# Kernel tuning notes

Measured on AMD Instinct MI355X. Metric: run time of the kernel, lower is better.

## Reference

```python
import jax, jax.numpy as jnp
import numpy as np

B, S_SPARSE, N_NUM, VOCAB = 512, 7, 6, 100
D, H, DFF, L = 1024, 16, 4096, 4
DH = D // 2  # 512, numeric encoding width
HD = D // H  # head dim 64
EPS = 1e-5


def setup_inputs() -> dict:
    key = jax.random.key(0)
    ks = jax.random.split(key, 16)
    inp = {
        'sparse': jax.random.randint(ks[0], (B, S_SPARSE), 0, VOCAB, dtype=jnp.int64),
        'numeric': jax.random.randint(ks[1], (B, N_NUM), 0, 100000, dtype=jnp.int32),
        'sparse_emb': jax.random.normal(ks[2], (VOCAB, D), jnp.float32),
        'numeric_emb': jax.random.normal(ks[3], (N_NUM, DH), jnp.float32),
        'Wqkv': jax.random.normal(ks[4], (L, 3 * D, D), jnp.float32) * 0.02,
        'bqkv': jnp.zeros((L, 3 * D), jnp.float32),
        'Wo': jax.random.normal(ks[5], (L, D, D), jnp.float32) * 0.02,
        'bo': jnp.zeros((L, D), jnp.float32),
        'W1': jax.random.normal(ks[6], (L, DFF, D), jnp.float32) * 0.02,
        'b1': jnp.zeros((L, DFF), jnp.float32),
        'W2': jax.random.normal(ks[7], (L, D, DFF), jnp.float32) * 0.02,
        'b2': jnp.zeros((L, D), jnp.float32),
        'ln1_g': jnp.ones((L, D), jnp.float32), 'ln1_b': jnp.zeros((L, D), jnp.float32),
        'ln2_g': jnp.ones((L, D), jnp.float32), 'ln2_b': jnp.zeros((L, D), jnp.float32),
    }
    return inp


def _ln(x, g, b):
    m = jnp.mean(x, -1, keepdims=True)
    v = jnp.mean((x - m) ** 2, -1, keepdims=True)
    return (x - m) * jax.lax.rsqrt(v + EPS) * g + b


def _encode_numeric(numeric):
    # piecewise-linear (thermometer) encoding, vectorized over batch & features
    mins = jnp.zeros((N_NUM,), jnp.float32)
    maxs = jnp.array([DH, DH, 100000.0, 100000.0, 100000.0, 100000.0], jnp.float32)
    scaled = (numeric.astype(jnp.float32) - mins) / (maxs - mins) * DH  # [B, 6]
    return jnp.clip(scaled[..., None] - jnp.arange(DH, dtype=jnp.float32), 0.0, 1.0)  # [B,6,DH]


def reference(sparse, numeric, sparse_emb, numeric_emb, Wqkv, bqkv, Wo, bo,
              W1, b1, W2, b2, ln1_g, ln1_b, ln2_g, ln2_b):
    enc = _encode_numeric(numeric)  # [B,6,DH]
    num_tok = jnp.concatenate(
        [enc, jnp.broadcast_to(numeric_emb[None], (sparse.shape[0], N_NUM, DH))], axis=2)  # [B,6,D]
    x = jnp.concatenate([sparse_emb[sparse], num_tok], axis=1)  # [B,13,D]

    scale = 1.0 / np.sqrt(HD)
    for l in range(L):
        qkv = jnp.einsum('bsd,ed->bse', x, Wqkv[l]) + bqkv[l]
        q, k, v = jnp.split(qkv, 3, axis=-1)
        bsz, s = x.shape[0], x.shape[1]
        q = q.reshape(bsz, s, H, HD)
        k = k.reshape(bsz, s, H, HD)
        v = v.reshape(bsz, s, H, HD)
        attn = jax.nn.softmax(jnp.einsum('bqhd,bkhd->bhqk', q, k) * scale, axis=-1)
        o = jnp.einsum('bhqk,bkhd->bqhd', attn, v).reshape(bsz, s, D)
        o = jnp.einsum('bsd,ed->bse', o, Wo[l]) + bo[l]
        x = _ln(x + o, ln1_g[l], ln1_b[l])  # post-norm
        h = jax.nn.gelu(jnp.einsum('bsd,fd->bsf', x, W1[l]) + b1[l], approximate=False)
        ff = jnp.einsum('bsf,df->bsd', h, W2[l]) + b2[l]
        x = _ln(x + ff, ln2_g[l], ln2_b[l])
    return x
```

## Files before the change

### kernel.cpp

```cpp
#include <hip/hip_runtime.h>
#include <hip/hip_bf16.h>
#include <cstdint>
#include <cmath>


typedef __bf16 bf16x8 __attribute__((ext_vector_type(8)));
typedef float  f32x4  __attribute__((ext_vector_type(4)));

__device__ __forceinline__ void async16(void* lds, const void* g) {
  __builtin_amdgcn_global_load_lds(
      (const __attribute__((address_space(1))) unsigned int*)g,
      (__attribute__((address_space(3))) unsigned int*)lds, 16, 0, 0);
}

__global__ __launch_bounds__(256) void f2b_kernel(const float* __restrict__ s,
                                                  __bf16* __restrict__ d, int n8) {
  int i = blockIdx.x * 256 + threadIdx.x;
  if (i >= n8) return;
  const float4* s4 = (const float4*)s;
  float4 a = s4[2 * i], b = s4[2 * i + 1];
  bf16x8 o;
  o[0] = (__bf16)a.x; o[1] = (__bf16)a.y; o[2] = (__bf16)a.z; o[3] = (__bf16)a.w;
  o[4] = (__bf16)b.x; o[5] = (__bf16)b.y; o[6] = (__bf16)b.z; o[7] = (__bf16)b.w;
  *(bf16x8*)(d + (size_t)i * 8) = o;
}

__global__ __launch_bounds__(256) void f2b2_kernel(
    const float* __restrict__ s0, __bf16* __restrict__ d0, int n0,
    const float* __restrict__ s1, __bf16* __restrict__ d1, int n8) {
  int i = blockIdx.x * 256 + threadIdx.x;
  if (i >= n8) return;
  const float* s; __bf16* d; int j;
  if (i < n0) { s = s0; d = d0; j = i; } else { s = s1; d = d1; j = i - n0; }
  const float4* s4 = (const float4*)s;
  float4 a = s4[2 * j], b = s4[2 * j + 1];
  bf16x8 o;
  o[0] = (__bf16)a.x; o[1] = (__bf16)a.y; o[2] = (__bf16)a.z; o[3] = (__bf16)a.w;
  o[4] = (__bf16)b.x; o[5] = (__bf16)b.y; o[6] = (__bf16)b.z; o[7] = (__bf16)b.w;
  *(bf16x8*)(d + (size_t)j * 8) = o;
}

__global__ __launch_bounds__(256) void build_x_kernel(
    const int* __restrict__ sparse, const int* __restrict__ numeric,
    const float* __restrict__ semb, const float* __restrict__ nemb,
    float* __restrict__ xf, __bf16* __restrict__ xb) {
  int r = blockIdx.x;
  int b = r / 13, s = r % 13;
  int t = threadIdx.x;
  size_t base = (size_t)r * 1024;
  if (s < 7) {
    int tok = sparse[b * 7 + s];
    const float* src = semb + (size_t)tok * 1024;
    for (int d = t; d < 1024; d += 256) {
      float v = src[d];
      xf[base + d] = v; xb[base + d] = (__bf16)v;
    }
  } else {
    int j = s - 7;
    float nv = (float)numeric[b * 6 + j];
    float scaled = nv * (j < 2 ? 1.0f : 512.0f / 100000.0f);
    for (int d = t; d < 1024; d += 256) {
      float v;
      if (d < 512) v = fminf(fmaxf(scaled - (float)d, 0.0f), 1.0f);
      else         v = nemb[j * 512 + (d - 512)];
      xf[base + d] = v; xb[base + d] = (__bf16)v;
    }
  }
}

template <int EPI>
__global__ __launch_bounds__(256) void gemm_bt(
    const __bf16* __restrict__ A, const __bf16* __restrict__ Bw,
    const float* __restrict__ bias, float* __restrict__ Cf,
    __bf16* __restrict__ Cb, int N, int K) {
  __shared__ __attribute__((aligned(16))) __bf16 As[128 * 64];
  __shared__ __attribute__((aligned(16))) __bf16 Bs[128 * 64];
  const int t = threadIdx.x;
  const int bm = blockIdx.x, bn = blockIdx.y;
  const int lane = t & 63, wid = t >> 6;
  const int wm = (wid >> 1) << 6, wn = (wid & 1) << 6;
  const int lm = lane & 15, lq = lane >> 4;
  const int srow = t >> 3, sp = t & 7;
  const int sc = sp ^ (srow & 7);
  const __bf16* Ag = A + (size_t)(bm * 128 + srow) * K + sc * 8;
  const __bf16* Bg = Bw + (size_t)(bn * 128 + srow) * K + sc * 8;
  const size_t rstep = (size_t)32 * K;
  f32x4 acc[4][4] = {};
  const int nIter = K >> 6;
  for (int k0 = 0; k0 < nIter; ++k0) {
    __syncthreads();
#pragma unroll
    for (int r = 0; r < 4; ++r) {
      async16(As + r * 2048 + t * 8, Ag + r * rstep);
      async16(Bs + r * 2048 + t * 8, Bg + r * rstep);
    }
    Ag += 64; Bg += 64;
    asm volatile("s_waitcnt vmcnt(0)" ::: "memory");
    __syncthreads();
#pragma unroll
    for (int kk = 0; kk < 2; ++kk) {
      bf16x8 af[4], bf[4];
#pragma unroll
      for (int i = 0; i < 4; i++) {
        int row = wm + i * 16 + lm;
        int pc = ((kk << 2) + lq) ^ (lm & 7);
        af[i] = *(const bf16x8*)(As + row * 64 + pc * 8);
      }
#pragma unroll
      for (int i = 0; i < 4; i++) {
        int row = wn + i * 16 + lm;
        int pc = ((kk << 2) + lq) ^ (lm & 7);
        bf[i] = *(const bf16x8*)(Bs + row * 64 + pc * 8);
      }
#pragma unroll
      for (int mi = 0; mi < 4; mi++)
#pragma unroll
        for (int ni = 0; ni < 4; ni++)
          acc[mi][ni] = __builtin_amdgcn_mfma_f32_16x16x32_bf16(af[mi], bf[ni], acc[mi][ni], 0, 0, 0);
    }
  }
  const int row0 = bm * 128 + wm + lq * 4;
  const int col0 = bn * 128 + wn + lm;
#pragma unroll
  for (int mi = 0; mi < 4; mi++) {
#pragma unroll
    for (int ni = 0; ni < 4; ni++) {
      int col = col0 + ni * 16;
      float bv = bias[col];
#pragma unroll
      for (int r = 0; r < 4; r++) {
        int row = row0 + mi * 16 + r;
        float v = acc[mi][ni][r] + bv;
        if (EPI == 2) {
          float u = fabsf(v);
          float y = 0.7978845608f * u * (1.0f + 0.044715f * u * u);
          float e = __expf(-2.0f * y);
          float th = (1.0f - e) * __builtin_amdgcn_rcpf(1.0f + e);
          v = 0.5f * v * (1.0f + (v < 0.0f ? -th : th));
        }
        if (EPI == 0) Cf[(size_t)row * N + col] = v;
        else          Cb[(size_t)row * N + col] = (__bf16)v;
      }
    }
  }
}

__global__ __launch_bounds__(64) void attn_kernel(const __bf16* __restrict__ qkv,
                                                  __bf16* __restrict__ o) {
  int bh = blockIdx.x;
  int b = bh >> 4, h = bh & 15;
  int lane = threadIdx.x;
  __shared__ float qs[13][68], ks[13][68], vs[13][68];
  __shared__ float S[13][16];
  const __bf16* base = qkv + (size_t)b * 13 * 3072 + h * 64 + lane;
#pragma unroll
  for (int i = 0; i < 13; i++) {
    qs[i][lane] = (float)base[(size_t)i * 3072];
    ks[i][lane] = (float)base[(size_t)i * 3072 + 1024];
    vs[i][lane] = (float)base[(size_t)i * 3072 + 2048];
  }
  __syncthreads();
  for (int rep = 0; rep < 3; rep++) {
    int idx = lane + rep * 64;
    if (idx < 169) {
      int i = idx / 13, j = idx % 13;
      float s = 0.f;
#pragma unroll
      for (int d = 0; d < 64; d++) s += qs[i][d] * ks[j][d];
      S[i][j] = s * 0.125f;
    }
  }
  __syncthreads();
  if (lane < 13) {
    float m = S[lane][0];
#pragma unroll
    for (int j = 1; j < 13; j++) m = fmaxf(m, S[lane][j]);
    float sum = 0.f;
#pragma unroll
    for (int j = 0; j < 13; j++) { float e = expf(S[lane][j] - m); S[lane][j] = e; sum += e; }
    float inv = 1.0f / sum;
#pragma unroll
    for (int j = 0; j < 13; j++) S[lane][j] *= inv;
  }
  __syncthreads();
  __bf16* ob = o + (size_t)b * 13 * 1024 + h * 64 + lane;
#pragma unroll
  for (int i = 0; i < 13; i++) {
    float s = 0.f;
#pragma unroll
    for (int j = 0; j < 13; j++) s += S[i][j] * vs[j][lane];
    ob[(size_t)i * 1024] = (__bf16)s;
  }
}

__global__ __launch_bounds__(256) void add_ln_kernel(
    const float* __restrict__ xin, const float* __restrict__ delta,
    const float* __restrict__ g, const float* __restrict__ bta,
    float* __restrict__ xf_out, __bf16* __restrict__ xb_out) {
  int r = blockIdx.x, t = threadIdx.x;
  size_t base = (size_t)r * 1024;
  float vals[4], s = 0.f, s2 = 0.f;
#pragma unroll
  for (int i = 0; i < 4; i++) {
    int d = t + i * 256;
    float v = xin[base + d] + delta[base + d];
    vals[i] = v; s += v; s2 += v * v;
  }
  __shared__ float red[8];
  for (int off = 32; off > 0; off >>= 1) { s += __shfl_down(s, off); s2 += __shfl_down(s2, off); }
  if ((t & 63) == 0) { red[t >> 6] = s; red[4 + (t >> 6)] = s2; }
  __syncthreads();
  float S1 = red[0] + red[1] + red[2] + red[3];
  float S2 = red[4] + red[5] + red[6] + red[7];
  float mean = S1 * (1.0f / 1024.0f);
  float var  = S2 * (1.0f / 1024.0f) - mean * mean;
  float inv  = rsqrtf(var + 1e-5f);
#pragma unroll
  for (int i = 0; i < 4; i++) {
    int d = t + i * 256;
    float y = (vals[i] - mean) * inv * g[d] + bta[d];
    xf_out[base + d] = y;
    xb_out[base + d] = (__bf16)y;
  }
}

extern "C" void kernel_launch(void* const* d_in, const int* in_sizes, int n_in,
                              void* d_out, int out_size, void* d_ws, size_t ws_size,
                              hipStream_t stream) {
  const int*   sparse  = (const int*)d_in[0];
  const int*   numeric = (const int*)d_in[1];
  const float* semb    = (const float*)d_in[2];
  const float* nemb    = (const float*)d_in[3];
  const float* Wqkv    = (const float*)d_in[4];
  const float* bqkv    = (const float*)d_in[5];
  const float* Wo      = (const float*)d_in[6];
  const float* bo      = (const float*)d_in[7];
  const float* W1      = (const float*)d_in[8];
  const float* b1      = (const float*)d_in[9];
  const float* W2      = (const float*)d_in[10];
  const float* b2      = (const float*)d_in[11];
  const float* ln1g    = (const float*)d_in[12];
  const float* ln1b    = (const float*)d_in[13];
  const float* ln2g    = (const float*)d_in[14];
  const float* ln2b    = (const float*)d_in[15];
  float* out = (float*)d_out;

  char* ws = (char*)d_ws;
  size_t off = 0;
  auto carve = [&](size_t bytes) -> char* {
    char* p = ws + off; off += (bytes + 255) & ~(size_t)255; return p;
  };
  __bf16* wb   = (__bf16*)carve((size_t)4096 * 1024 * 2);
  float*  xf   = (float*) carve((size_t)6656 * 1024 * 4);
  __bf16* xb   = (__bf16*)carve((size_t)6656 * 1024 * 2);
  char*   pool = carve((size_t)6656 * 4096 * 2);
  __bf16* qkvb  = (__bf16*)pool;
  __bf16* attnb = (__bf16*)(pool + (size_t)6656 * 3072 * 2);
  __bf16* hb    = (__bf16*)pool;
  float*  tmpf  = out;

  build_x_kernel<<<6656, 256, 0, stream>>>(sparse, numeric, semb, nemb, xf, xb);

  for (int l = 0; l < 4; ++l) {
    f2b2_kernel<<<2048, 256, 0, stream>>>(Wqkv + (size_t)l * 3145728, wb, 393216,
                                          Wo + (size_t)l * 1048576, wb + 3145728, 524288);
    gemm_bt<1><<<dim3(52, 24), 256, 0, stream>>>(xb, wb, bqkv + l * 3072, nullptr, qkvb, 3072, 1024);
    attn_kernel<<<8192, 64, 0, stream>>>(qkvb, attnb);
    gemm_bt<0><<<dim3(52, 8), 256, 0, stream>>>(attnb, wb + 3145728, bo + l * 1024, tmpf, nullptr, 1024, 1024);
    add_ln_kernel<<<6656, 256, 0, stream>>>(xf, tmpf, ln1g + l * 1024, ln1b + l * 1024, xf, xb);
    f2b_kernel<<<2048, 256, 0, stream>>>(W1 + (size_t)l * 4194304, wb, 524288);
    gemm_bt<2><<<dim3(52, 32), 256, 0, stream>>>(xb, wb, b1 + l * 4096, nullptr, hb, 4096, 1024);
    f2b_kernel<<<2048, 256, 0, stream>>>(W2 + (size_t)l * 4194304, wb, 524288);
    gemm_bt<0><<<dim3(52, 8), 256, 0, stream>>>(hb, wb, b2 + l * 1024, tmpf, nullptr, 1024, 4096);
    float* xdst = (l == 3) ? out : xf;
    add_ln_kernel<<<6656, 256, 0, stream>>>(xf, tmpf, ln2g + l * 1024, ln2b + l * 1024, xdst, xb);
  }
}
```

Baseline: 1.439 ms.

## Split GEMM into wide 128x256 and narrow 64x128 tile variants

Replaces the single 128x128-tile GEMM with two specialised kernels. For the wide-N projections (QKV, FFN1), a 128x256 tile uses 4 waves that each cover all 128 rows and 64 columns, which raises reuse of the A tile. For the N=1024 projections (Wo, FFN2), a 64x128 tile with 128 threads doubles the block count to 832, so the grid fills the GPU better. The wide kernel needs more accumulator registers (32 f32x4 per thread) and 48KB of LDS, which can limit occupancy despite the launch bounds hint.

```diff
diff --git a/kernel.cpp b/kernel.cpp
--- a/kernel.cpp
+++ b/kernel.cpp
@@ -11,6 +11,14 @@
   __builtin_amdgcn_global_load_lds(
       (const __attribute__((address_space(1))) unsigned int*)g,
       (__attribute__((address_space(3))) unsigned int*)lds, 16, 0, 0);
+}
+
+__device__ __forceinline__ float gelu_f(float v) {
+  float u = fabsf(v);
+  float y = 0.7978845608f * u * (1.0f + 0.044715f * u * u);
+  float e = __expf(-2.0f * y);
+  float th = (1.0f - e) * __builtin_amdgcn_rcpf(1.0f + e);
+  return 0.5f * v * (1.0f + (v < 0.0f ? -th : th));
 }
 
 __global__ __launch_bounds__(256) void f2b_kernel(const float* __restrict__ s,
@@ -69,49 +77,100 @@
 }
 
 template <int EPI>
-__global__ __launch_bounds__(256) void gemm_bt(
+__global__ __launch_bounds__(256, 2) void gemm_wide(
     const __bf16* __restrict__ A, const __bf16* __restrict__ Bw,
-    const float* __restrict__ bias, float* __restrict__ Cf,
-    __bf16* __restrict__ Cb, int N, int K) {
+    const float* __restrict__ bias, __bf16* __restrict__ Cb, int N, int K) {
   __shared__ __attribute__((aligned(16))) __bf16 As[128 * 64];
+  __shared__ __attribute__((aligned(16))) __bf16 Bs[256 * 64];
+  const int t = threadIdx.x;
+  const int bm = blockIdx.x, bn = blockIdx.y;
+  const int lane = t & 63, wid = t >> 6;
+  const int wn = wid << 6;
+  const int lm = lane & 15, lq = lane >> 4;
+  const int srow = t >> 3, sp = t & 7;
+  const int sc = sp ^ (srow & 7);
+  const __bf16* Ag = A + (size_t)(bm * 128 + srow) * K + sc * 8;
+  const __bf16* Bg = Bw + (size_t)(bn * 256 + srow) * K + sc * 8;
+  const size_t rstep = (size_t)32 * K;
+  f32x4 acc[8][4] = {};
+  const int nIter = K >> 6;
+  for (int k0 = 0; k0 < nIter; ++k0) {
+    __syncthreads();
+#pragma unroll
+    for (int r = 0; r < 4; ++r) async16(As + r * 2048 + t * 8, Ag + r * rstep);
+#pragma unroll
+    for (int r = 0; r < 8; ++r) async16(Bs + r * 2048 + t * 8, Bg + r * rstep);
+    Ag += 64; Bg += 64;
+    asm volatile("s_waitcnt vmcnt(0)" ::: "memory");
+    __syncthreads();
+#pragma unroll
+    for (int kk = 0; kk < 2; ++kk) {
+      const int pc = ((kk << 2) + lq) ^ (lm & 7);
+      bf16x8 af[8], bf[4];
+#pragma unroll
+      for (int i = 0; i < 8; i++) af[i] = *(const bf16x8*)(As + (i * 16 + lm) * 64 + pc * 8);
+#pragma unroll
+      for (int i = 0; i < 4; i++) bf[i] = *(const bf16x8*)(Bs + (wn + i * 16 + lm) * 64 + pc * 8);
+#pragma unroll
+      for (int mi = 0; mi < 8; mi++)
+#pragma unroll
+        for (int ni = 0; ni < 4; ni++)
+          acc[mi][ni] = __builtin_amdgcn_mfma_f32_16x16x32_bf16(af[mi], bf[ni], acc[mi][ni], 0, 0, 0);
+    }
+  }
+  const int row0 = bm * 128 + lq * 4;
+  const int col0 = bn * 256 + wn + lm;
+#pragma unroll
+  for (int mi = 0; mi < 8; mi++) {
+#pragma unroll
+    for (int ni = 0; ni < 4; ni++) {
+      int col = col0 + ni * 16;
+      float bv = bias[col];
+#pragma unroll
+      for (int r = 0; r < 4; r++) {
+        int row = row0 + mi * 16 + r;
+        float v = acc[mi][ni][r] + bv;
+        if (EPI == 2) v = gelu_f(v);
+        Cb[(size_t)row * N + col] = (__bf16)v;
+      }
+    }
+  }
+}
+
+__global__ __launch_bounds__(128, 4) void gemm_narrow(
+    const __bf16* __restrict__ A, const __bf16* __restrict__ Bw,
+    const float* __restrict__ bias, float* __restrict__ Cf, int N, int K) {
+  __shared__ __attribute__((aligned(16))) __bf16 As[64 * 64];
   __shared__ __attribute__((aligned(16))) __bf16 Bs[128 * 64];
   const int t = threadIdx.x;
   const int bm = blockIdx.x, bn = blockIdx.y;
   const int lane = t & 63, wid = t >> 6;
-  const int wm = (wid >> 1) << 6, wn = (wid & 1) << 6;
+  const int wn = wid << 6;
   const int lm = lane & 15, lq = lane >> 4;
   const int srow = t >> 3, sp = t & 7;
   const int sc = sp ^ (srow & 7);
-  const __bf16* Ag = A + (size_t)(bm * 128 + srow) * K + sc * 8;
+  const __bf16* Ag = A + (size_t)(bm * 64 + srow) * K + sc * 8;
   const __bf16* Bg = Bw + (size_t)(bn * 128 + srow) * K + sc * 8;
-  const size_t rstep = (size_t)32 * K;
+  const size_t rstep = (size_t)16 * K;
   f32x4 acc[4][4] = {};
   const int nIter = K >> 6;
   for (int k0 = 0; k0 < nIter; ++k0) {
     __syncthreads();
 #pragma unroll
-    for (int r = 0; r < 4; ++r) {
-      async16(As + r * 2048 + t * 8, Ag + r * rstep);
-      async16(Bs + r * 2048 + t * 8, Bg + r * rstep);
-    }
+    for (int r = 0; r < 4; ++r) async16(As + r * 1024 + t * 8, Ag + r * rstep);
+#pragma unroll
+    for (int r = 0; r < 8; ++r) async16(Bs + r * 1024 + t * 8, Bg + r * rstep);
     Ag += 64; Bg += 64;
     asm volatile("s_waitcnt vmcnt(0)" ::: "memory");
     __syncthreads();
 #pragma unroll
     for (int kk = 0; kk < 2; ++kk) {
+      const int pc = ((kk << 2) + lq) ^ (lm & 7);
       bf16x8 af[4], bf[4];
 #pragma unroll
-      for (int i = 0; i < 4; i++) {
-        int row = wm + i * 16 + lm;
-        int pc = ((kk << 2) + lq) ^ (lm & 7);
-        af[i] = *(const bf16x8*)(As + row * 64 + pc * 8);
-      }
-#pragma unroll
-      for (int i = 0; i < 4; i++) {
-        int row = wn + i * 16 + lm;
-        int pc = ((kk << 2) + lq) ^ (lm & 7);
-        bf[i] = *(const bf16x8*)(Bs + row * 64 + pc * 8);
-      }
+      for (int i = 0; i < 4; i++) af[i] = *(const bf16x8*)(As + (i * 16 + lm) * 64 + pc * 8);
+#pragma unroll
+      for (int i = 0; i < 4; i++) bf[i] = *(const bf16x8*)(Bs + (wn + i * 16 + lm) * 64 + pc * 8);
 #pragma unroll
       for (int mi = 0; mi < 4; mi++)
 #pragma unroll
@@ -119,7 +178,7 @@
           acc[mi][ni] = __builtin_amdgcn_mfma_f32_16x16x32_bf16(af[mi], bf[ni], acc[mi][ni], 0, 0, 0);
     }
   }
-  const int row0 = bm * 128 + wm + lq * 4;
+  const int row0 = bm * 64 + lq * 4;
   const int col0 = bn * 128 + wn + lm;
 #pragma unroll
   for (int mi = 0; mi < 4; mi++) {
@@ -130,16 +189,7 @@
 #pragma unroll
       for (int r = 0; r < 4; r++) {
         int row = row0 + mi * 16 + r;
-        float v = acc[mi][ni][r] + bv;
-        if (EPI == 2) {
-          float u = fabsf(v);
-          float y = 0.7978845608f * u * (1.0f + 0.044715f * u * u);
-          float e = __expf(-2.0f * y);
-          float th = (1.0f - e) * __builtin_amdgcn_rcpf(1.0f + e);
-          v = 0.5f * v * (1.0f + (v < 0.0f ? -th : th));
-        }
-        if (EPI == 0) Cf[(size_t)row * N + col] = v;
-        else          Cb[(size_t)row * N + col] = (__bf16)v;
+        Cf[(size_t)row * N + col] = acc[mi][ni][r] + bv;
       }
     }
   }
@@ -264,14 +314,14 @@
   for (int l = 0; l < 4; ++l) {
     f2b2_kernel<<<2048, 256, 0, stream>>>(Wqkv + (size_t)l * 3145728, wb, 393216,
                                           Wo + (size_t)l * 1048576, wb + 3145728, 524288);
-    gemm_bt<1><<<dim3(52, 24), 256, 0, stream>>>(xb, wb, bqkv + l * 3072, nullptr, qkvb, 3072, 1024);
+    gemm_wide<1><<<dim3(52, 12), 256, 0, stream>>>(xb, wb, bqkv + l * 3072, qkvb, 3072, 1024);
     attn_kernel<<<8192, 64, 0, stream>>>(qkvb, attnb);
-    gemm_bt<0><<<dim3(52, 8), 256, 0, stream>>>(attnb, wb + 3145728, bo + l * 1024, tmpf, nullptr, 1024, 1024);
+    gemm_narrow<<<dim3(104, 8), 128, 0, stream>>>(attnb, wb + 3145728, bo + l * 1024, tmpf, 1024, 1024);
     add_ln_kernel<<<6656, 256, 0, stream>>>(xf, tmpf, ln1g + l * 1024, ln1b + l * 1024, xf, xb);
     f2b_kernel<<<2048, 256, 0, stream>>>(W1 + (size_t)l * 4194304, wb, 524288);
-    gemm_bt<2><<<dim3(52, 32), 256, 0, stream>>>(xb, wb, b1 + l * 4096, nullptr, hb, 4096, 1024);
+    gemm_wide<2><<<dim3(52, 16), 256, 0, stream>>>(xb, wb, b1 + l * 4096, hb, 4096, 1024);
     f2b_kernel<<<2048, 256, 0, stream>>>(W2 + (size_t)l * 4194304, wb, 524288);
-    gemm_bt<0><<<dim3(52, 8), 256, 0, stream>>>(hb, wb, b2 + l * 1024, tmpf, nullptr, 1024, 4096);
+    gemm_narrow<<<dim3(104, 8), 128, 0, stream>>>(hb, wb, b2 + l * 1024, tmpf, 1024, 4096);
     float* xdst = (l == 3) ? out : xf;
     add_ln_kernel<<<6656, 256, 0, stream>>>(xf, tmpf, ln2g + l * 1024, ln2b + l * 1024, xdst, xb);
   }
```

New measurement: 1.383 ms. -3.9%, faster.
